# Kernel optimization log

Measured on AMD Instinct MI355X. Metric: run time of the kernel, lower is better.

The kernel has to match this reference:

```python
import jax, jax.numpy as jnp
import numpy as np

N = 100000   # nodes
D = 64       # in_features
E = 1200000  # edges (avg degree ~12)
C = 1.0      # curvature
MIN_NORM = 1e-15
PROJ_EPS = 4e-3  # float32 eps used by HGCN-style PoincareBall.proj


def setup_inputs() -> dict:
    key = jax.random.key(0)
    k1, k2, k3 = jax.random.split(key, 3)
    x = jax.random.normal(k1, (N, D), dtype=jnp.float32) * 0.1
    edge_index = jax.random.randint(k2, (2, E), 0, N, dtype=jnp.int32)
    # GCNConv learned params (lin weight + bias)
    W = jax.random.normal(k3, (D, D), dtype=jnp.float32) / np.sqrt(D)
    b = jnp.zeros((D,), dtype=jnp.float32)
    return {"x": x, "W": W, "b": b, "edge_index": edge_index}


def expmap0(u, c):
    sqrt_c = jnp.sqrt(c)
    u_norm = jnp.maximum(jnp.linalg.norm(u, axis=-1, keepdims=True), MIN_NORM)
    return jnp.tanh(sqrt_c * u_norm) * u / (sqrt_c * u_norm)


def proj(x, c):
    norm = jnp.maximum(jnp.linalg.norm(x, axis=-1, keepdims=True), MIN_NORM)
    maxnorm = (1.0 - PROJ_EPS) / jnp.sqrt(c)
    return jnp.where(norm > maxnorm, x / norm * maxnorm, x)


def gcn_conv(x, W, b, edge_index, n_nodes):
    # PyG GCNConv: h = x @ W; add self-loops; symmetric normalization; scatter-add; + bias
    h = x @ W  # [N, D]
    src, dst = edge_index[0], edge_index[1]
    loops = jnp.arange(n_nodes, dtype=edge_index.dtype)
    s = jnp.concatenate([src, loops])  # [E+N]
    d = jnp.concatenate([dst, loops])
    deg = jax.ops.segment_sum(jnp.ones(s.shape, dtype=h.dtype), d, num_segments=n_nodes)
    deg_inv_sqrt = jnp.where(deg > 0, deg ** -0.5, 0.0)
    norm = deg_inv_sqrt[s] * deg_inv_sqrt[d]  # [E+N]
    msgs = h[s] * norm[:, None]               # gather + scale: [E+N, D]
    out = jax.ops.segment_sum(msgs, d, num_segments=n_nodes)  # scatter-add
    return out + b


def reference(x, W, b, edge_index):
    # Note: original computes logmap0(x) but discards it (conv uses raw x) -- dead code.
    support_t = gcn_conv(x, W, b, edge_index, N)
    return proj(expmap0(support_t, C), C)
```

## Files before the change

### kernel.cpp

```cpp
#include <hip/hip_runtime.h>
#include <hip/hip_bf16.h>

#define DFEAT 64
#define NBSH  8
#define NPB   256
#define EPB   8192

__global__ __launch_bounds__(256) void histA_kernel(const int* __restrict__ ei,
                                                    int* __restrict__ blkhistT,
                                                    int E, int nblk) {
    __shared__ int h[512];
    int t = threadIdx.x;
    h[t] = 0; h[t + 256] = 0;
    __syncthreads();
    int base = blockIdx.x * EPB;
    #pragma unroll
    for (int i = 0; i < EPB / 256; ++i) {
        int e = base + i * 256 + t;
        if (e < E) atomicAdd(&h[ei[E + e] >> NBSH], 1);
    }
    __syncthreads();
    blkhistT[t * nblk + blockIdx.x]         = h[t];
    blkhistT[(t + 256) * nblk + blockIdx.x] = h[t + 256];
}

__global__ __launch_bounds__(256) void scanB1_kernel(int* __restrict__ blkhistT,
                                                     int* __restrict__ buckettotal, int nblk) {
    __shared__ int lds[256];
    int t = threadIdx.x;
    int b = blockIdx.x;
    int v = (t < nblk) ? blkhistT[b * nblk + t] : 0;
    lds[t] = v;
    __syncthreads();
    #pragma unroll
    for (int off = 1; off < 256; off <<= 1) {
        int y = (t >= off) ? lds[t - off] : 0;
        __syncthreads();
        lds[t] += y;
        __syncthreads();
    }
    if (t < nblk) blkhistT[b * nblk + t] = lds[t] - v;
    if (t == 255) buckettotal[b] = lds[255];
}

__global__ __launch_bounds__(512) void scanB2_kernel(const int* __restrict__ buckettotal,
                                                     int* __restrict__ bucketbase) {
    __shared__ int lds[512];
    int t = threadIdx.x;
    int s = buckettotal[t];
    lds[t] = s;
    __syncthreads();
    #pragma unroll
    for (int off = 1; off < 512; off <<= 1) {
        int y = (t >= off) ? lds[t - off] : 0;
        __syncthreads();
        lds[t] += y;
        __syncthreads();
    }
    bucketbase[t] = lds[t] - s;
    if (t == 511) bucketbase[512] = lds[511];
}

__global__ __launch_bounds__(256) void partC_kernel(const int* __restrict__ ei,
                                                    const int* __restrict__ blkhistT,
                                                    const int* __restrict__ bucketbase,
                                                    unsigned* __restrict__ ebuf, int E, int nblk) {
    __shared__ int cur[512];
    int t = threadIdx.x;
    cur[t]       = bucketbase[t]       + blkhistT[t * nblk + blockIdx.x];
    cur[t + 256] = bucketbase[t + 256] + blkhistT[(t + 256) * nblk + blockIdx.x];
    __syncthreads();
    int base = blockIdx.x * EPB;
    #pragma unroll
    for (int i = 0; i < EPB / 256; ++i) {
        int e = base + i * 256 + t;
        if (e < E) {
            int s = ei[e];
            int d = ei[E + e];
            int pos = atomicAdd(&cur[d >> NBSH], 1);
            ebuf[pos] = (unsigned)s | ((unsigned)(d & (NPB - 1)) << 17);
        }
    }
}

__global__ __launch_bounds__(256) void csrD_kernel(const unsigned* __restrict__ ebuf,
                                                   const int* __restrict__ bucketbase,
                                                   int* __restrict__ srcs,
                                                   int* __restrict__ begs,
                                                   int* __restrict__ lens,
                                                   float* __restrict__ dinv, int n) {
    __shared__ int cnt[256];
    __shared__ int tmp[256];
    int t = threadIdx.x;
    int b = blockIdx.x;
    int ebeg = bucketbase[b], eend = bucketbase[b + 1];
    int regionbase = ebeg + b * (4 * NPB);
    cnt[t] = 0;
    __syncthreads();
    for (int e = ebeg + t; e < eend; e += 256)
        atomicAdd(&cnt[ebuf[e] >> 17], 1);
    __syncthreads();
    int nid = (b << NBSH) + t;
    int deg = cnt[t];
    int slots = (nid < n) ? ((deg + 4) & ~3) : 0;
    tmp[t] = slots;
    __syncthreads();
    int s = slots;
    for (int o = 1; o < 256; o <<= 1) {
        int y = (t >= o) ? tmp[t - o] : 0;
        __syncthreads();
        tmp[t] += y;
        __syncthreads();
    }
    int excl = tmp[t] - s;
    if (nid < n) {
        int beg_abs = regionbase + excl;
        begs[nid] = beg_abs;
        lens[nid] = slots;
        dinv[nid] = rsqrtf((float)(deg + 1));
        srcs[beg_abs] = nid;
        for (int k = deg + 1; k < slots; ++k) srcs[beg_abs + k] = n;
    }
    cnt[t] = excl + 1;
    __syncthreads();
    for (int e = ebeg + t; e < eend; e += 256) {
        unsigned v = ebuf[e];
        int pos = atomicAdd(&cnt[v >> 17], 1);
        srcs[regionbase + pos] = (int)(v & 0x1ffffu);
    }
}

__global__ __launch_bounds__(256) void xsprep_kernel(const float* __restrict__ x,
                                                     const float* __restrict__ dinv,
                                                     unsigned* __restrict__ xs, int n) {
    int i = blockIdx.x * blockDim.x + threadIdx.x;
    int total = (n + 1) * 32;
    if (i >= total) return;
    int row = i >> 5, col = i & 31;
    unsigned v = 0;
    if (row < n) {
        float di = dinv[row];
        float f0 = x[row * DFEAT + 2 * col] * di;
        float f1 = x[row * DFEAT + 2 * col + 1] * di;
        unsigned u0 = __float_as_uint(f0); u0 = (u0 + 0x7fffu + ((u0 >> 16) & 1u)) >> 16;
        unsigned u1 = __float_as_uint(f1); u1 = (u1 + 0x7fffu + ((u1 >> 16) & 1u)) >> 16;
        v = (u0 & 0xffffu) | (u1 << 16);
    }
    xs[i] = v;
}

__global__ __launch_bounds__(256) void agg_kernel(const int* __restrict__ begs,
                                                  const int* __restrict__ lens,
                                                  const int* __restrict__ srcs,
                                                  const float* __restrict__ dinv,
                                                  const uint2* __restrict__ xs2,
                                                  const float* __restrict__ W,
                                                  const float* __restrict__ b,
                                                  float* __restrict__ out,
                                                  int n, int noctets) {
    __shared__ float Wl[DFEAT * DFEAT];
    __shared__ float xl[8][DFEAT];
    int t = threadIdx.x;
    #pragma unroll
    for (int i = 0; i < 16; ++i) Wl[i * 256 + t] = W[i * 256 + t];
    __syncthreads();

    int r = t >> 6, lane = t & 63;
    int g = lane >> 4;
    int q = lane & 15;
    float bias = b[lane];

    for (int oct = blockIdx.x; oct < noctets; oct += gridDim.x) {
        int na = oct * 8 + r;
        int nb_ = na + 4;
        bool va = na < n, vb = nb_ < n;
        if (!va) continue;

        int beg0 = begs[na],  end0 = beg0 + lens[na];
        int beg1 = 0, end1 = 0;
        if (vb) { beg1 = begs[nb_]; end1 = beg1 + lens[nb_]; }

        float a0 = 0, a1 = 0, a2 = 0, a3 = 0;
        float b0 = 0, b1 = 0, b2 = 0, b3 = 0;
        int base0 = beg0, base1 = beg1;
        while (base0 < end0 || base1 < end1) {
            int m0 = end0 - base0; m0 = m0 < 0 ? 0 : (m0 > 64 ? 64 : m0);
            int m1 = end1 - base1; m1 = m1 < 0 ? 0 : (m1 > 64 ? 64 : m1);
            int idx0 = 0, idx1 = 0;
            if (lane < m0) idx0 = srcs[base0 + lane];
            if (lane < m1) idx1 = srcs[base1 + lane];
            int q0 = m0 >> 2, q1 = m1 >> 2;
            int qc = q0 < q1 ? q0 : q1;
            #pragma unroll 4
            for (int j = 0; j < qc; ++j) {
                int sv0 = __shfl(idx0, 4 * j + g, 64);
                int sv1 = __shfl(idx1, 4 * j + g, 64);
                uint2 d0 = xs2[(unsigned)sv0 * 16 + q];
                uint2 d1 = xs2[(unsigned)sv1 * 16 + q];
                a0 += __uint_as_float(d0.x << 16);
                a1 += __uint_as_float(d0.x & 0xffff0000u);
                a2 += __uint_as_float(d0.y << 16);
                a3 += __uint_as_float(d0.y & 0xffff0000u);
                b0 += __uint_as_float(d1.x << 16);
                b1 += __uint_as_float(d1.x & 0xffff0000u);
                b2 += __uint_as_float(d1.y << 16);
                b3 += __uint_as_float(d1.y & 0xffff0000u);
            }
            #pragma unroll 4
            for (int j = qc; j < q0; ++j) {
                int sv0 = __shfl(idx0, 4 * j + g, 64);
                uint2 d0 = xs2[(unsigned)sv0 * 16 + q];
                a0 += __uint_as_float(d0.x << 16);
                a1 += __uint_as_float(d0.x & 0xffff0000u);
                a2 += __uint_as_float(d0.y << 16);
                a3 += __uint_as_float(d0.y & 0xffff0000u);
            }
            #pragma unroll 4
            for (int j = qc; j < q1; ++j) {
                int sv1 = __shfl(idx1, 4 * j + g, 64);
                uint2 d1 = xs2[(unsigned)sv1 * 16 + q];
                b0 += __uint_as_float(d1.x << 16);
                b1 += __uint_as_float(d1.x & 0xffff0000u);
                b2 += __uint_as_float(d1.y << 16);
                b3 += __uint_as_float(d1.y & 0xffff0000u);
            }
            base0 += 64; base1 += 64;
        }
        #pragma unroll
        for (int off = 16; off < 64; off <<= 1) {
            a0 += __shfl_xor(a0, off, 64);
            a1 += __shfl_xor(a1, off, 64);
            a2 += __shfl_xor(a2, off, 64);
            a3 += __shfl_xor(a3, off, 64);
            b0 += __shfl_xor(b0, off, 64);
            b1 += __shfl_xor(b1, off, 64);
            b2 += __shfl_xor(b2, off, 64);
            b3 += __shfl_xor(b3, off, 64);
        }
        if (g == 0) {
            float dia = dinv[na];
            xl[r][4 * q + 0] = a0 * dia;
            xl[r][4 * q + 1] = a1 * dia;
            xl[r][4 * q + 2] = a2 * dia;
            xl[r][4 * q + 3] = a3 * dia;
            if (vb) {
                float dib = dinv[nb_];
                xl[r + 4][4 * q + 0] = b0 * dib;
                xl[r + 4][4 * q + 1] = b1 * dib;
                xl[r + 4][4 * q + 2] = b2 * dib;
                xl[r + 4][4 * q + 3] = b3 * dib;
            }
        }

        float oa0 = bias, oa1 = 0.0f, ob0 = bias, ob1 = 0.0f;
        #pragma unroll
        for (int k = 0; k < DFEAT; k += 2) {
            float w0 = Wl[k * DFEAT + lane];
            float w1 = Wl[(k + 1) * DFEAT + lane];
            oa0 = fmaf(xl[r][k],     w0, oa0);
            oa1 = fmaf(xl[r][k + 1], w1, oa1);
            ob0 = fmaf(xl[r + 4][k],     w0, ob0);
            ob1 = fmaf(xl[r + 4][k + 1], w1, ob1);
        }
        float oa = oa0 + oa1;
        float ob = ob0 + ob1;

        float ssa = oa * oa, ssb = ob * ob;
        #pragma unroll
        for (int off = 32; off > 0; off >>= 1) {
            ssa += __shfl_xor(ssa, off, 64);
            ssb += __shfl_xor(ssb, off, 64);
        }
        float norma = fmaxf(sqrtf(ssa), 1e-15f);
        float sca = fminf(tanhf(norma), 1.0f - 4e-3f) / norma;
        out[(long long)na * DFEAT + lane] = oa * sca;
        if (vb) {
            float normb = fmaxf(sqrtf(ssb), 1e-15f);
            float scb = fminf(tanhf(normb), 1.0f - 4e-3f) / normb;
            out[(long long)nb_ * DFEAT + lane] = ob * scb;
        }
    }
}


extern "C" void kernel_launch(void* const* d_in, const int* in_sizes, int n_in,
                              void* d_out, int out_size, void* d_ws, size_t ws_size,
                              hipStream_t stream) {
    const float* x = (const float*)d_in[0];
    const float* W = (const float*)d_in[1];
    const float* b = (const float*)d_in[2];
    const int* ei  = (const int*)d_in[3];

    int n = in_sizes[0] / DFEAT;
    int E = in_sizes[3] / 2;
    int NB = (n + NPB - 1) / NPB;
    int nblk = (E + EPB - 1) / EPB;
    int noctets = (n + 7) / 8;

    int* blkhistT    = (int*)d_ws;
    int* buckettotal = blkhistT + 512 * nblk;
    int* bucketbase  = buckettotal + 512;
    int* srcs        = bucketbase + 516;
    int* begs        = srcs + E + NB * 4 * NPB;
    int* lens        = begs + n;
    float* dinv      = (float*)(lens + n);
    size_t xsoff     = (size_t)(((int*)dinv + n) - (int*)d_ws);
    xsoff            = (xsoff + 31) & ~(size_t)31;
    unsigned* xs     = (unsigned*)d_ws + xsoff;
    unsigned* ebuf   = xs + (size_t)(n + 1) * 32;

    float* out = (float*)d_out;

    int aggblocks = 2048;
    if (aggblocks > noctets) aggblocks = noctets;

    histA_kernel <<<nblk, 256, 0, stream>>>(ei, blkhistT, E, nblk);
    scanB1_kernel<<<512, 256, 0, stream>>>(blkhistT, buckettotal, nblk);
    scanB2_kernel<<<1, 512, 0, stream>>>(buckettotal, bucketbase);
    partC_kernel <<<nblk, 256, 0, stream>>>(ei, blkhistT, bucketbase, ebuf, E, nblk);
    csrD_kernel  <<<NB, 256, 0, stream>>>(ebuf, bucketbase, srcs, begs, lens, dinv, n);
    xsprep_kernel<<<((n + 1) * 32 + 255) / 256, 256, 0, stream>>>(x, dinv, xs, n);
    agg_kernel   <<<aggblocks, 256, 0, stream>>>(begs, lens, srcs, dinv,
                                                 (const uint2*)xs, W, b, out, n, noctets);
}
```

Before: 190.7 us.

## Replace bucketed CSR build with global-atomic degree count and scatter

```diff
diff --git a/kernel.cpp b/kernel.cpp
--- a/kernel.cpp
+++ b/kernel.cpp
@@ -2,107 +2,26 @@
 #include <hip/hip_bf16.h>
 
 #define DFEAT 64
-#define NBSH  8
-#define NPB   256
-#define EPB   8192
-
-__global__ __launch_bounds__(256) void histA_kernel(const int* __restrict__ ei,
-                                                    int* __restrict__ blkhistT,
-                                                    int E, int nblk) {
-    __shared__ int h[512];
+
+__global__ __launch_bounds__(256) void deg_kernel(const int* __restrict__ ei,
+                                                  int* __restrict__ deg, int E) {
+    int e = blockIdx.x * 256 + threadIdx.x;
+    if (e < E) atomicAdd(&deg[ei[E + e]], 1);
+}
+
+__global__ __launch_bounds__(256) void alloc_kernel(const int* __restrict__ deg,
+                                                    int* __restrict__ alloc,
+                                                    int* __restrict__ begs,
+                                                    int* __restrict__ lens,
+                                                    int* __restrict__ cur,
+                                                    float* __restrict__ dinv,
+                                                    int* __restrict__ srcs, int n) {
+    __shared__ int tmp[256];
+    __shared__ int basesh;
     int t = threadIdx.x;
-    h[t] = 0; h[t + 256] = 0;
-    __syncthreads();
-    int base = blockIdx.x * EPB;
-    #pragma unroll
-    for (int i = 0; i < EPB / 256; ++i) {
-        int e = base + i * 256 + t;
-        if (e < E) atomicAdd(&h[ei[E + e] >> NBSH], 1);
-    }
-    __syncthreads();
-    blkhistT[t * nblk + blockIdx.x]         = h[t];
-    blkhistT[(t + 256) * nblk + blockIdx.x] = h[t + 256];
-}
-
-__global__ __launch_bounds__(256) void scanB1_kernel(int* __restrict__ blkhistT,
-                                                     int* __restrict__ buckettotal, int nblk) {
-    __shared__ int lds[256];
-    int t = threadIdx.x;
-    int b = blockIdx.x;
-    int v = (t < nblk) ? blkhistT[b * nblk + t] : 0;
-    lds[t] = v;
-    __syncthreads();
-    #pragma unroll
-    for (int off = 1; off < 256; off <<= 1) {
-        int y = (t >= off) ? lds[t - off] : 0;
-        __syncthreads();
-        lds[t] += y;
-        __syncthreads();
-    }
-    if (t < nblk) blkhistT[b * nblk + t] = lds[t] - v;
-    if (t == 255) buckettotal[b] = lds[255];
-}
-
-__global__ __launch_bounds__(512) void scanB2_kernel(const int* __restrict__ buckettotal,
-                                                     int* __restrict__ bucketbase) {
-    __shared__ int lds[512];
-    int t = threadIdx.x;
-    int s = buckettotal[t];
-    lds[t] = s;
-    __syncthreads();
-    #pragma unroll
-    for (int off = 1; off < 512; off <<= 1) {
-        int y = (t >= off) ? lds[t - off] : 0;
-        __syncthreads();
-        lds[t] += y;
-        __syncthreads();
-    }
-    bucketbase[t] = lds[t] - s;
-    if (t == 511) bucketbase[512] = lds[511];
-}
-
-__global__ __launch_bounds__(256) void partC_kernel(const int* __restrict__ ei,
-                                                    const int* __restrict__ blkhistT,
-                                                    const int* __restrict__ bucketbase,
-                                                    unsigned* __restrict__ ebuf, int E, int nblk) {
-    __shared__ int cur[512];
-    int t = threadIdx.x;
-    cur[t]       = bucketbase[t]       + blkhistT[t * nblk + blockIdx.x];
-    cur[t + 256] = bucketbase[t + 256] + blkhistT[(t + 256) * nblk + blockIdx.x];
-    __syncthreads();
-    int base = blockIdx.x * EPB;
-    #pragma unroll
-    for (int i = 0; i < EPB / 256; ++i) {
-        int e = base + i * 256 + t;
-        if (e < E) {
-            int s = ei[e];
-            int d = ei[E + e];
-            int pos = atomicAdd(&cur[d >> NBSH], 1);
-            ebuf[pos] = (unsigned)s | ((unsigned)(d & (NPB - 1)) << 17);
-        }
-    }
-}
-
-__global__ __launch_bounds__(256) void csrD_kernel(const unsigned* __restrict__ ebuf,
-                                                   const int* __restrict__ bucketbase,
-                                                   int* __restrict__ srcs,
-                                                   int* __restrict__ begs,
-                                                   int* __restrict__ lens,
-                                                   float* __restrict__ dinv, int n) {
-    __shared__ int cnt[256];
-    __shared__ int tmp[256];
-    int t = threadIdx.x;
-    int b = blockIdx.x;
-    int ebeg = bucketbase[b], eend = bucketbase[b + 1];
-    int regionbase = ebeg + b * (4 * NPB);
-    cnt[t] = 0;
-    __syncthreads();
-    for (int e = ebeg + t; e < eend; e += 256)
-        atomicAdd(&cnt[ebuf[e] >> 17], 1);
-    __syncthreads();
-    int nid = (b << NBSH) + t;
-    int deg = cnt[t];
-    int slots = (nid < n) ? ((deg + 4) & ~3) : 0;
+    int nid = blockIdx.x * 256 + t;
+    int d = (nid < n) ? deg[nid] : 0;
+    int slots = (nid < n) ? ((d + 4) & ~3) : 0;
     tmp[t] = slots;
     __syncthreads();
     int s = slots;
@@ -112,26 +31,22 @@
         tmp[t] += y;
         __syncthreads();
     }
+    if (t == 255) basesh = atomicAdd(alloc, tmp[255]);
     int excl = tmp[t] - s;
+    __syncthreads();
+    int beg = basesh + excl;
     if (nid < n) {
-        int beg_abs = regionbase + excl;
-        begs[nid] = beg_abs;
+        begs[nid] = beg;
         lens[nid] = slots;
-        dinv[nid] = rsqrtf((float)(deg + 1));
-        srcs[beg_abs] = nid;
-        for (int k = deg + 1; k < slots; ++k) srcs[beg_abs + k] = n;
-    }
-    cnt[t] = excl + 1;
-    __syncthreads();
-    for (int e = ebeg + t; e < eend; e += 256) {
-        unsigned v = ebuf[e];
-        int pos = atomicAdd(&cnt[v >> 17], 1);
-        srcs[regionbase + pos] = (int)(v & 0x1ffffu);
+        cur[nid]  = beg + 1;
+        dinv[nid] = rsqrtf((float)(d + 1));
+        srcs[beg] = nid;
+        for (int k = d + 1; k < slots; ++k) srcs[beg + k] = n;
     }
 }
 
 __global__ __launch_bounds__(256) void xsprep_kernel(const float* __restrict__ x,
-                                                     const float* __restrict__ dinv,
+                                                     const int* __restrict__ deg,
                                                      unsigned* __restrict__ xs, int n) {
     int i = blockIdx.x * blockDim.x + threadIdx.x;
     int total = (n + 1) * 32;
@@ -139,7 +54,7 @@
     int row = i >> 5, col = i & 31;
     unsigned v = 0;
     if (row < n) {
-        float di = dinv[row];
+        float di = rsqrtf((float)(deg[row] + 1));
         float f0 = x[row * DFEAT + 2 * col] * di;
         float f1 = x[row * DFEAT + 2 * col + 1] * di;
         unsigned u0 = __float_as_uint(f0); u0 = (u0 + 0x7fffu + ((u0 >> 16) & 1u)) >> 16;
@@ -147,6 +62,18 @@
         v = (u0 & 0xffffu) | (u1 << 16);
     }
     xs[i] = v;
+}
+
+__global__ __launch_bounds__(256) void scat_kernel(const int* __restrict__ ei,
+                                                   int* __restrict__ cur,
+                                                   int* __restrict__ srcs, int E) {
+    int e = blockIdx.x * 256 + threadIdx.x;
+    if (e < E) {
+        int s = ei[e];
+        int d = ei[E + e];
+        int pos = atomicAdd(&cur[d], 1);
+        srcs[pos] = s;
+    }
 }
 
 __global__ __launch_bounds__(256) void agg_kernel(const int* __restrict__ begs,
@@ -293,33 +220,31 @@
 
     int n = in_sizes[0] / DFEAT;
     int E = in_sizes[3] / 2;
-    int NB = (n + NPB - 1) / NPB;
-    int nblk = (E + EPB - 1) / EPB;
+    int NB = (n + 255) / 256;
     int noctets = (n + 7) / 8;
 
-    int* blkhistT    = (int*)d_ws;
-    int* buckettotal = blkhistT + 512 * nblk;
-    int* bucketbase  = buckettotal + 512;
-    int* srcs        = bucketbase + 516;
-    int* begs        = srcs + E + NB * 4 * NPB;
-    int* lens        = begs + n;
-    float* dinv      = (float*)(lens + n);
-    size_t xsoff     = (size_t)(((int*)dinv + n) - (int*)d_ws);
-    xsoff            = (xsoff + 31) & ~(size_t)31;
-    unsigned* xs     = (unsigned*)d_ws + xsoff;
-    unsigned* ebuf   = xs + (size_t)(n + 1) * 32;
+    int* deg   = (int*)d_ws;
+    int* alloc = deg + n;
+    int* begs  = alloc + 4;
+    int* lens  = begs + n;
+    int* cur   = lens + n;
+    float* dinv = (float*)(cur + n);
+    int* srcs  = (int*)(dinv + n);
+    size_t srcs_cap = (size_t)E + 4 * (size_t)n;
+    size_t xsoff = (size_t)((srcs + srcs_cap) - (int*)d_ws);
+    xsoff = (xsoff + 31) & ~(size_t)31;
+    unsigned* xs = (unsigned*)d_ws + xsoff;
 
     float* out = (float*)d_out;
 
     int aggblocks = 2048;
     if (aggblocks > noctets) aggblocks = noctets;
 
-    histA_kernel <<<nblk, 256, 0, stream>>>(ei, blkhistT, E, nblk);
-    scanB1_kernel<<<512, 256, 0, stream>>>(blkhistT, buckettotal, nblk);
-    scanB2_kernel<<<1, 512, 0, stream>>>(buckettotal, bucketbase);
-    partC_kernel <<<nblk, 256, 0, stream>>>(ei, blkhistT, bucketbase, ebuf, E, nblk);
-    csrD_kernel  <<<NB, 256, 0, stream>>>(ebuf, bucketbase, srcs, begs, lens, dinv, n);
-    xsprep_kernel<<<((n + 1) * 32 + 255) / 256, 256, 0, stream>>>(x, dinv, xs, n);
+    hipMemsetAsync(deg, 0, (size_t)(n + 4) * sizeof(int), stream);
+    deg_kernel   <<<(E + 255) / 256, 256, 0, stream>>>(ei, deg, E);
+    alloc_kernel <<<NB, 256, 0, stream>>>(deg, alloc, begs, lens, cur, dinv, srcs, n);
+    xsprep_kernel<<<((n + 1) * 32 + 255) / 256, 256, 0, stream>>>(x, deg, xs, n);
+    scat_kernel  <<<(E + 255) / 256, 256, 0, stream>>>(ei, cur, srcs, E);
     agg_kernel   <<<aggblocks, 256, 0, stream>>>(begs, lens, srcs, dinv,
                                                  (const uint2*)xs, W, b, out, n, noctets);
 }
```

Result: slower. 301.5 us (+58.1%).
